# Performance work log

Hardware: AMD Instinct MI355X
Metric: run time of the kernel (lower is better)

The kernel has to match this reference:

```python
import jax, jax.numpy as jnp
import numpy as np

D_MODEL = 1024
D = 512
B = 32
L = 1024


def setup_inputs() -> dict:
    key = jax.random.key(0)
    ks = jax.random.split(key, 8)
    s = 1.0 / np.sqrt(D_MODEL)
    x = jax.random.normal(ks[0], (B, L, D_MODEL), dtype=jnp.float32)
    mask = jnp.ones((B, 1, L), dtype=jnp.int32)  # padding mask; 1 = keep
    Wq = jax.random.uniform(ks[1], (D, D_MODEL), jnp.float32, -s, s)
    bq = jax.random.uniform(ks[2], (D,), jnp.float32, -s, s)
    Wk = jax.random.uniform(ks[3], (D, D_MODEL), jnp.float32, -s, s)
    bk = jax.random.uniform(ks[4], (D,), jnp.float32, -s, s)
    Wv = jax.random.uniform(ks[5], (D, D_MODEL), jnp.float32, -s, s)
    bv = jax.random.uniform(ks[6], (D,), jnp.float32, -s, s)
    return {"x": x, "Wq": Wq, "bq": bq, "Wk": Wk, "bk": bk, "Wv": Wv, "bv": bv, "mask": mask}


def reference(x, Wq, bq, Wk, bk, Wv, bv, mask):
    Bq, Lq, _ = x.shape
    q = jnp.einsum('blc,dc->bld', x, Wq) + bq  # [B,L,D]
    k = jnp.einsum('blc,dc->bld', x, Wk) + bk
    v = jnp.einsum('blc,dc->bld', x, Wv) + bv
    scale = k.shape[-1] ** -0.5
    weights = jnp.einsum('bid,bjd->bij', q, k) * scale  # [B,L,L]
    causal = jnp.tril(jnp.ones((Lq, Lq), dtype=bool))
    neg_inf = jnp.float32(-jnp.inf)
    weights = jnp.where(causal[None, :, :], weights, neg_inf)
    weights = jnp.where(mask == 0, neg_inf, weights)  # mask broadcasts [B,1,L]
    weights = jax.nn.softmax(weights, axis=-1)
    # NOTE: source calls self.dropout(weights) but discards result -> no-op
    out = jnp.einsum('bij,bjd->bid', weights, v)
    return jax.nn.relu(out)
```

## Files before the change

### kernel.cpp

```cpp
#include <hip/hip_runtime.h>
#include <hip/hip_bf16.h>
#include <stdint.h>

#define DM 1024
#define DD 512
#define BB 32
#define LL 1024
#define SCALE 0.04419417382415922f
#define MAT ((size_t)BB * LL * DD)

typedef float f32x4 __attribute__((ext_vector_type(4)));
typedef short bf16x8 __attribute__((ext_vector_type(8)));
typedef short bf16x4 __attribute__((ext_vector_type(4)));

__device__ inline unsigned short f2bf(float f) {
    union { float f; uint32_t u; } v; v.f = f;
    uint32_t r = v.u + 0x7fffu + ((v.u >> 16) & 1u);
    return (unsigned short)(r >> 16);
}

__device__ inline bf16x4 cvt4(f32x4 a, float s) {
    bf16x4 r;
    r[0] = (short)f2bf(a[0] * s);
    r[1] = (short)f2bf(a[1] * s);
    r[2] = (short)f2bf(a[2] * s);
    r[3] = (short)f2bf(a[3] * s);
    return r;
}

#define GLOAD_LDS16(gsrc, ldst) \
    __builtin_amdgcn_global_load_lds((const __attribute__((address_space(1))) unsigned int*)(gsrc), \
        (__attribute__((address_space(3))) unsigned int*)(ldst), 16, 0, 0)

__device__ inline void tile_barrier() {
    asm volatile("s_waitcnt vmcnt(0)" ::: "memory");
    __builtin_amdgcn_sched_barrier(0);
    __builtin_amdgcn_s_barrier();
    __builtin_amdgcn_sched_barrier(0);
}

__global__ __launch_bounds__(256) void cast_x(const float* __restrict__ x,
                                              unsigned short* __restrict__ xb)
{
    size_t idx = (size_t)blockIdx.x * 256 + threadIdx.x;
    size_t base = idx * 8;
    f32x4 a = *(const f32x4*)(x + base);
    f32x4 b = *(const f32x4*)(x + base + 4);
    bf16x4 lo = cvt4(a, 1.0f), hi = cvt4(b, 1.0f);
    bf16x8 o = {lo[0], lo[1], lo[2], lo[3], hi[0], hi[1], hi[2], hi[3]};
    *(bf16x8*)(xb + base) = o;
}

__global__ __launch_bounds__(256) void cast_w(const float* __restrict__ Wq,
                                              const float* __restrict__ Wk,
                                              const float* __restrict__ Wv,
                                              unsigned short* __restrict__ Wb)
{
    size_t idx = (size_t)blockIdx.x * 256 + threadIdx.x;
    int o = (int)(idx >> 16);
    size_t rem = idx & 65535;
    const float* W = (o == 0) ? Wq : (o == 1) ? Wk : Wv;
    float s = (o == 0) ? SCALE : 1.0f;
    size_t base = rem * 8;
    f32x4 a = *(const f32x4*)(W + base);
    f32x4 b = *(const f32x4*)(W + base + 4);
    bf16x4 lo = cvt4(a, s), hi = cvt4(b, s);
    bf16x8 out = {lo[0], lo[1], lo[2], lo[3], hi[0], hi[1], hi[2], hi[3]};
    *(bf16x8*)(Wb + (size_t)o * 524288 + base) = out;
}

__global__ __launch_bounds__(256, 2) void qkv_proj3(
    const unsigned short* __restrict__ xb,
    const unsigned short* __restrict__ Wb,
    const float* __restrict__ bq, const float* __restrict__ bk, const float* __restrict__ bv,
    unsigned short* __restrict__ qkv)
{
    __shared__ __align__(16) unsigned short At[2][8192];
    __shared__ __align__(16) unsigned short Bt[2][8192];

    const int o = blockIdx.y;
    const float* bias = (o == 0) ? bq : (o == 1) ? bk : bv;
    const float wscale = (o == 0) ? SCALE : 1.0f;
    const unsigned short* W = Wb + (size_t)o * 524288;
    unsigned short* out = qkv + (size_t)o * MAT;

    int wg = blockIdx.x;
    wg = (wg & 7) * 128 + (wg >> 3);
    const int rowbase = (wg >> 2) * 128;
    const int colbase = (wg & 3) * 128;

    const int tid  = threadIdx.x;
    const int lane = tid & 63;
    const int w    = tid >> 6;
    const int wr   = (w >> 1) * 64;
    const int wc   = (w & 1) * 64;
    const int l15  = lane & 15, l4 = lane >> 4;

    const int r8   = lane >> 3;
    const int swch = (lane & 7) ^ r8;

    const char* xpanel = (const char*)(xb + (size_t)rowbase * DM);
    const char* wpanel = (const char*)(W  + (size_t)colbase * DM);

    f32x4 acc[4][4];
    #pragma unroll
    for (int i = 0; i < 4; ++i)
        #pragma unroll
        for (int j = 0; j < 4; ++j)
            acc[i][j] = (f32x4){0.f, 0.f, 0.f, 0.f};

    #define STAGE_AB(KK, BUF) do {                                               \
        _Pragma("unroll")                                                        \
        for (int i2 = 0; i2 < 4; ++i2) {                                         \
            int grp = i2 * 4 + w;                 \
            size_t rowoff = (size_t)(grp * 8 + r8) * 2048 + (KK) * 2 + swch * 16;\
            GLOAD_LDS16(xpanel + rowoff, (char*)&At[BUF][0] + grp * 1024);       \
            GLOAD_LDS16(wpanel + rowoff, (char*)&Bt[BUF][0] + grp * 1024);       \
        }                                                                        \
    } while (0)

    STAGE_AB(0, 0);
    __syncthreads();

    for (int t = 0; t < 16; ++t) {
        const int cur = t & 1;
        if (t < 15) STAGE_AB((t + 1) * 64, cur ^ 1);

        const char* Ab = (const char*)&At[cur][0];
        const char* Bb = (const char*)&Bt[cur][0];
        #pragma unroll
        for (int ks = 0; ks < 2; ++ks) {
            bf16x8 af[4], bf_[4];
            const int ch = (ks * 4 + l4) ^ (l15 & 7);
            #pragma unroll
            for (int m = 0; m < 4; ++m) {
                int row = wr + m * 16 + l15;
                af[m] = *(const bf16x8*)(Ab + row * 128 + (ch << 4));
            }
            #pragma unroll
            for (int n = 0; n < 4; ++n) {
                int row = wc + n * 16 + l15;
                bf_[n] = *(const bf16x8*)(Bb + row * 128 + (ch << 4));
            }
            #pragma unroll
            for (int n = 0; n < 4; ++n)
                #pragma unroll
                for (int m = 0; m < 4; ++m)
                    acc[m][n] = __builtin_amdgcn_mfma_f32_16x16x32_bf16(af[m], bf_[n], acc[m][n], 0, 0, 0);
        }

        if (t < 15) tile_barrier();
    }
    #undef STAGE_AB

    #pragma unroll
    for (int n = 0; n < 4; ++n) {
        int col = colbase + wc + n * 16 + l15;
        float bv_ = bias[col] * wscale;
        #pragma unroll
        for (int m = 0; m < 4; ++m) {
            int row0 = rowbase + wr + m * 16 + l4 * 4;
            #pragma unroll
            for (int r = 0; r < 4; ++r)
                out[(size_t)(row0 + r) * DD + col] = f2bf(acc[m][n][r] + bv_);
        }
    }
}

__global__ __launch_bounds__(256) void vtrans(const unsigned short* __restrict__ v,
                                              unsigned short* __restrict__ vt)
{
    __shared__ unsigned short T[64][72];
    const int lt = blockIdx.x, dt = blockIdx.y, b = blockIdx.z;
    const int t = threadIdx.x;
    const unsigned short* src = v + ((size_t)(b * LL + lt * 64)) * DD + dt * 64;
    #pragma unroll
    for (int it = 0; it < 2; ++it) {
        int r  = (t >> 3) + it * 32;
        int c0 = (t & 7) * 8;
        bf16x8 x = *(const bf16x8*)(src + (size_t)r * DD + c0);
        *(bf16x4*)&T[r][c0]     = (bf16x4){x[0], x[1], x[2], x[3]};
        *(bf16x4*)&T[r][c0 + 4] = (bf16x4){x[4], x[5], x[6], x[7]};
    }
    __syncthreads();
    unsigned short* dst = vt + ((size_t)(b * DD + dt * 64)) * LL + lt * 64;
    #pragma unroll
    for (int it = 0; it < 2; ++it) {
        int d  = (t >> 3) + it * 32;
        int c0 = (t & 7) * 8;
        bf16x8 o;
        #pragma unroll
        for (int e = 0; e < 8; ++e) o[e] = T[c0 + e][d];
        *(bf16x8*)(dst + (size_t)d * LL + c0) = o;
    }
}

__global__ __launch_bounds__(256, 1) void attn3(
    const unsigned short* __restrict__ qkv,
    const unsigned short* __restrict__ vt,
    const int* __restrict__ mask,
    float* __restrict__ outp)
{
    __shared__ __align__(16) unsigned short KtL[2][16384];
    __shared__ __align__(16) unsigned short VtL[2][16384];
    __shared__ __align__(16) unsigned short Pw[4][16][36];
    __shared__ float mbias[1024];

    const int bx = blockIdx.x;
    const int h = bx >> 8, i = bx & 255;
    const int b = i & 31;
    const int qtx = (i >> 5) & 7;
    const int qt = h ? qtx : 15 - qtx;

    const int tid = threadIdx.x, lane = tid & 63, w = tid >> 6;
    const int l15 = lane & 15, l4 = lane >> 4;
    const int lsw = lane * 16;

    const unsigned short* q = qkv;
    const unsigned short* k = qkv + MAT;
    const char* kb  = (const char*)k + ((size_t)b * LL) * DD * 2;
    const char* vtb = (const char*)vt + ((size_t)b * DD) * LL * 2;

    {
        const int* mp = mask + b * LL;
        #pragma unroll
        for (int j = 0; j < 4; ++j)
            mbias[tid * 4 + j] = mp[tid * 4 + j] ? 0.0f : -1e30f;
    }

    bf16x8 qf[16];
    {
        const unsigned short* qp = q + ((size_t)(b * LL + qt * 64 + w * 16 + l15)) * DD + l4 * 8;
        #pragma unroll
        for (int ks = 0; ks < 16; ++ks)
            qf[ks] = *(const bf16x8*)(qp + ks * 32);
    }

    f32x4 oacc[32];
    #pragma unroll
    for (int n = 0; n < 32; ++n) oacc[n] = (f32x4){0.f, 0.f, 0.f, 0.f};
    float mrow[4] = {-1e30f, -1e30f, -1e30f, -1e30f};
    float lrow[4] = {0.f, 0.f, 0.f, 0.f};

    const int jtmax = 2 * qt + 1;

    #define STAGE_KV(JT, BUF) do {                                              \
        const char* kt = kb + ((size_t)(JT) << 15);                             \
        char* ldsK = (char*)&KtL[(BUF)][0];                                     \
        _Pragma("unroll")                                                       \
        for (int i2 = 0; i2 < 8; ++i2) {                                        \
            int row = i2 * 4 + w;                                               \
            GLOAD_LDS16(kt + (row << 10) + (lsw ^ ((row & 7) << 4)),            \
                        ldsK + (row << 10));                                    \
        }                                                                       \
        const char* vtj = vtb + ((size_t)(JT) << 6);                            \
        char* ldsV = (char*)&VtL[(BUF)][0];                                     \
        _Pragma("unroll")                                                       \
        for (int i2 = 0; i2 < 8; ++i2) {                                        \
            int c0 = i2 * 256 + w * 64;                                         \
            int c  = c0 + lane;                                                 \
            GLOAD_LDS16(vtj + ((size_t)(c >> 2) << 11) + ((c & 3) << 4),        \
                        ldsV + c0 * 16);                                        \
        }                                                                       \
    } while (0)

    STAGE_KV(0, 0);
    __syncthreads();

    const int swz = (l15 & 7) << 4;

    for (int jt = 0; jt <= jtmax; ++jt) {
        const int cur = jt & 1;
        if (jt < jtmax) STAGE_KV(jt + 1, cur ^ 1);

        const char* Kc = (const char*)&KtL[cur][0];
        f32x4 sacc[2];
        sacc[0] = (f32x4){0.f, 0.f, 0.f, 0.f};
        sacc[1] = (f32x4){0.f, 0.f, 0.f, 0.f};
        #pragma unroll
        for (int ks = 0; ks < 16; ++ks) {
            int coloff = ((ks << 6) + (l4 << 4)) ^ swz;
            #pragma unroll
            for (int nf = 0; nf < 2; ++nf) {
                const bf16x8 kf = *(const bf16x8*)(Kc + ((nf * 16 + l15) << 10) + coloff);
                sacc[nf] = __builtin_amdgcn_mfma_f32_16x16x32_bf16(qf[ks], kf, sacc[nf], 0, 0, 0);
            }
        }

        const bool diag = (jt >= 2 * qt);
        float s[2][4];
        #pragma unroll
        for (int nf = 0; nf < 2; ++nf) {
            float bb_ = mbias[jt * 32 + nf * 16 + l15];
            #pragma unroll
            for (int r = 0; r < 4; ++r) {
                float val = sacc[nf][r] + bb_;
                if (diag) {
                    int gi = qt * 64 + w * 16 + l4 * 4 + r;
                    int gj = jt * 32 + nf * 16 + l15;
                    val = (gj <= gi) ? val : -3e38f;
                }
                s[nf][r] = val;
            }
        }
        float pm[4];
        #pragma unroll
        for (int r = 0; r < 4; ++r) {
            float mx = fmaxf(s[0][r], s[1][r]);
            mx = fmaxf(mx, __shfl_xor(mx, 1));
            mx = fmaxf(mx, __shfl_xor(mx, 2));
            mx = fmaxf(mx, __shfl_xor(mx, 4));
            mx = fmaxf(mx, __shfl_xor(mx, 8));
            pm[r] = mx;
        }
        bool need = false;
        #pragma unroll
        for (int r = 0; r < 4; ++r) need |= (pm[r] - mrow[r] > 8.0f);
        if (__any(need)) {
            #pragma unroll
            for (int r = 0; r < 4; ++r) {
                float mn = fmaxf(mrow[r], pm[r]);
                float corr = __expf(mrow[r] - mn);
                mrow[r] = mn;
                lrow[r] *= corr;
                #pragma unroll
                for (int n = 0; n < 32; ++n) oacc[n][r] *= corr;
            }
        }
        #pragma unroll
        for (int r = 0; r < 4; ++r) {
            float ls = 0.f;
            #pragma unroll
            for (int nf = 0; nf < 2; ++nf) {
                float p = __expf(s[nf][r] - mrow[r]);
                ls += p;
                Pw[w][l4 * 4 + r][nf * 16 + l15] = f2bf(p);
            }
            ls += __shfl_xor(ls, 1);
            ls += __shfl_xor(ls, 2);
            ls += __shfl_xor(ls, 4);
            ls += __shfl_xor(ls, 8);
            lrow[r] += ls;
        }

        const bf16x8 pa = *(const bf16x8*)&Pw[w][l15][l4 * 8];
        const char* Vc = (const char*)&VtL[cur][0];
        #pragma unroll
        for (int n = 0; n < 32; ++n) {
            const bf16x8 vb_ = *(const bf16x8*)(Vc + ((n * 16 + l15) << 6) + (l4 << 4));
            oacc[n] = __builtin_amdgcn_mfma_f32_16x16x32_bf16(pa, vb_, oacc[n], 0, 0, 0);
        }

        if (jt < jtmax) tile_barrier();
    }

    float inv[4];
    #pragma unroll
    for (int r = 0; r < 4; ++r) inv[r] = 1.0f / lrow[r];
    float* op = outp + ((size_t)(b * LL + qt * 64 + w * 16 + l4 * 4)) * DD + l15;
    #pragma unroll
    for (int n = 0; n < 32; ++n)
        #pragma unroll
        for (int r = 0; r < 4; ++r)
            op[(size_t)r * DD + n * 16] = fmaxf(oacc[n][r] * inv[r], 0.f);
    #undef STAGE_KV
}

extern "C" void kernel_launch(void* const* d_in, const int* in_sizes, int n_in,
                              void* d_out, int out_size, void* d_ws, size_t ws_size,
                              hipStream_t stream) {
    const float* x  = (const float*)d_in[0];
    const float* Wq = (const float*)d_in[1];
    const float* bq = (const float*)d_in[2];
    const float* Wk = (const float*)d_in[3];
    const float* bk = (const float*)d_in[4];
    const float* Wv = (const float*)d_in[5];
    const float* bv = (const float*)d_in[6];
    const int* mask = (const int*)d_in[7];

    unsigned short* qkv = (unsigned short*)d_ws;
    unsigned short* v   = qkv + 2 * MAT;
    unsigned short* vtp = qkv + 3 * MAT;
    unsigned short* Wb  = vtp;
    unsigned short* xb  = (unsigned short*)d_out;
    float* out = (float*)d_out;

    cast_x<<<16384, 256, 0, stream>>>(x, xb);
    cast_w<<<768, 256, 0, stream>>>(Wq, Wk, Wv, Wb);
    qkv_proj3<<<dim3(1024, 3), 256, 0, stream>>>(xb, Wb, bq, bk, bv, qkv);
    vtrans<<<dim3(16, 8, 32), 256, 0, stream>>>(v, vtp);
    attn3<<<dim3(512), 256, 0, stream>>>(qkv, vtp, mask, out);
}
```

Before: 290.8 us.

## Single-buffer K/V in LDS with staggered staging for two blocks per CU

The attention kernel drops its double-buffered K and V LDS tiles for single buffers, halving its LDS footprint. Launch bounds now request two blocks per CU, so all 512 blocks can be resident at once instead of running as two waves. To keep some overlap, the V tile is loaded while QK^T runs and the next K tile while P·V runs, with a barrier between phases. The risks are an extra barrier per iteration, lost intra-block prefetch depth, and possible register spills under the tighter per-wave VGPR budget.

```diff
diff --git a/kernel.cpp b/kernel.cpp
--- a/kernel.cpp
+++ b/kernel.cpp
@@ -32,7 +32,7 @@
     __builtin_amdgcn_global_load_lds((const __attribute__((address_space(1))) unsigned int*)(gsrc), \
         (__attribute__((address_space(3))) unsigned int*)(ldst), 16, 0, 0)
 
-__device__ inline void tile_barrier() {
+__device__ inline void publish_barrier() {
     asm volatile("s_waitcnt vmcnt(0)" ::: "memory");
     __builtin_amdgcn_sched_barrier(0);
     __builtin_amdgcn_s_barrier();
@@ -112,7 +112,7 @@
     #define STAGE_AB(KK, BUF) do {                                               \
         _Pragma("unroll")                                                        \
         for (int i2 = 0; i2 < 4; ++i2) {                                         \
-            int grp = i2 * 4 + w;                 \
+            int grp = i2 * 4 + w;                                                \
             size_t rowoff = (size_t)(grp * 8 + r8) * 2048 + (KK) * 2 + swch * 16;\
             GLOAD_LDS16(xpanel + rowoff, (char*)&At[BUF][0] + grp * 1024);       \
             GLOAD_LDS16(wpanel + rowoff, (char*)&Bt[BUF][0] + grp * 1024);       \
@@ -149,7 +149,7 @@
                     acc[m][n] = __builtin_amdgcn_mfma_f32_16x16x32_bf16(af[m], bf_[n], acc[m][n], 0, 0, 0);
         }
 
-        if (t < 15) tile_barrier();
+        if (t < 15) publish_barrier();
     }
     #undef STAGE_AB
 
@@ -195,14 +195,14 @@
     }
 }
 
-__global__ __launch_bounds__(256, 1) void attn3(
+__global__ __launch_bounds__(256, 2) void attn4(
     const unsigned short* __restrict__ qkv,
     const unsigned short* __restrict__ vt,
     const int* __restrict__ mask,
     float* __restrict__ outp)
 {
-    __shared__ __align__(16) unsigned short KtL[2][16384];
-    __shared__ __align__(16) unsigned short VtL[2][16384];
+    __shared__ __align__(16) unsigned short KtL[16384];
+    __shared__ __align__(16) unsigned short VtL[16384];
     __shared__ __align__(16) unsigned short Pw[4][16][36];
     __shared__ float mbias[1024];
 
@@ -244,36 +244,35 @@
 
     const int jtmax = 2 * qt + 1;
 
-    #define STAGE_KV(JT, BUF) do {                                              \
+    #define STAGE_K(JT) do {                                                    \
         const char* kt = kb + ((size_t)(JT) << 15);                             \
-        char* ldsK = (char*)&KtL[(BUF)][0];                                     \
         _Pragma("unroll")                                                       \
         for (int i2 = 0; i2 < 8; ++i2) {                                        \
             int row = i2 * 4 + w;                                               \
             GLOAD_LDS16(kt + (row << 10) + (lsw ^ ((row & 7) << 4)),            \
-                        ldsK + (row << 10));                                    \
+                        (char*)KtL + (row << 10));                              \
         }                                                                       \
+    } while (0)
+
+    #define STAGE_V(JT) do {                                                    \
         const char* vtj = vtb + ((size_t)(JT) << 6);                            \
-        char* ldsV = (char*)&VtL[(BUF)][0];                                     \
         _Pragma("unroll")                                                       \
         for (int i2 = 0; i2 < 8; ++i2) {                                        \
             int c0 = i2 * 256 + w * 64;                                         \
             int c  = c0 + lane;                                                 \
             GLOAD_LDS16(vtj + ((size_t)(c >> 2) << 11) + ((c & 3) << 4),        \
-                        ldsV + c0 * 16);                                        \
+                        (char*)VtL + c0 * 16);                                  \
         }                                                                       \
     } while (0)
 
-    STAGE_KV(0, 0);
-    __syncthreads();
+    STAGE_K(0);
 
     const int swz = (l15 & 7) << 4;
 
     for (int jt = 0; jt <= jtmax; ++jt) {
-        const int cur = jt & 1;
-        if (jt < jtmax) STAGE_KV(jt + 1, cur ^ 1);
-
-        const char* Kc = (const char*)&KtL[cur][0];
+        publish_barrier();
+        STAGE_V(jt);
+
         f32x4 sacc[2];
         sacc[0] = (f32x4){0.f, 0.f, 0.f, 0.f};
         sacc[1] = (f32x4){0.f, 0.f, 0.f, 0.f};
@@ -282,7 +281,7 @@
             int coloff = ((ks << 6) + (l4 << 4)) ^ swz;
             #pragma unroll
             for (int nf = 0; nf < 2; ++nf) {
-                const bf16x8 kf = *(const bf16x8*)(Kc + ((nf * 16 + l15) << 10) + coloff);
+                const bf16x8 kf = *(const bf16x8*)((const char*)KtL + ((nf * 16 + l15) << 10) + coloff);
                 sacc[nf] = __builtin_amdgcn_mfma_f32_16x16x32_bf16(qf[ks], kf, sacc[nf], 0, 0, 0);
             }
         }
@@ -343,15 +342,15 @@
             lrow[r] += ls;
         }
 
+        publish_barrier();
+        if (jt < jtmax) STAGE_K(jt + 1);
+
         const bf16x8 pa = *(const bf16x8*)&Pw[w][l15][l4 * 8];
-        const char* Vc = (const char*)&VtL[cur][0];
         #pragma unroll
         for (int n = 0; n < 32; ++n) {
-            const bf16x8 vb_ = *(const bf16x8*)(Vc + ((n * 16 + l15) << 6) + (l4 << 4));
+            const bf16x8 vb_ = *(const bf16x8*)((const char*)VtL + ((n * 16 + l15) << 6) + (l4 << 4));
             oacc[n] = __builtin_amdgcn_mfma_f32_16x16x32_bf16(pa, vb_, oacc[n], 0, 0, 0);
         }
-
-        if (jt < jtmax) tile_barrier();
     }
 
     float inv[4];
@@ -363,7 +362,8 @@
         #pragma unroll
         for (int r = 0; r < 4; ++r)
             op[(size_t)r * DD + n * 16] = fmaxf(oacc[n][r] * inv[r], 0.f);
-    #undef STAGE_KV
+    #undef STAGE_K
+    #undef STAGE_V
 }
 
 extern "C" void kernel_launch(void* const* d_in, const int* in_sizes, int n_in,
@@ -389,5 +389,5 @@
     cast_w<<<768, 256, 0, stream>>>(Wq, Wk, Wv, Wb);
     qkv_proj3<<<dim3(1024, 3), 256, 0, stream>>>(xb, Wb, bq, bk, bv, qkv);
     vtrans<<<dim3(16, 8, 32), 256, 0, stream>>>(v, vtp);
-    attn3<<<dim3(512), 256, 0, stream>>>(qkv, vtp, mask, out);
-}
+    attn4<<<dim3(512), 256, 0, stream>>>(qkv, vtp, mask, out);
+}
```

New measurement: 390.2 us. 34.2% more time.

## Restructure QKV projection into 256x256 tiles with 8 waves and staged half-tile pipeline

Applied to the files above, without the earlier changes.

Replaces the 128x128-tile, 4-wave QKV projection GEMM with a 256x256 tile computed by 8 waves, splitting each K-step's A and B panels into halves. The halves are loaded in a staggered order, gated by partial vmcnt waits and barriers, so MFMA work on one quarter of the output tile overlaps loads of the next K-step. The larger tile raises operand reuse and cuts global traffic per FLOP. The cost is more accumulator registers (32 f32x4 per thread), 64KB of LDS, fewer workgroups, and four barriers per iteration.

```diff
diff --git a/kernel.cpp b/kernel.cpp
--- a/kernel.cpp
+++ b/kernel.cpp
@@ -34,6 +34,36 @@
 
 __device__ inline void tile_barrier() {
     asm volatile("s_waitcnt vmcnt(0)" ::: "memory");
+    __builtin_amdgcn_sched_barrier(0);
+    __builtin_amdgcn_s_barrier();
+    __builtin_amdgcn_sched_barrier(0);
+}
+
+__device__ inline void gate6() {
+    asm volatile("s_waitcnt vmcnt(6)" ::: "memory");
+    __builtin_amdgcn_sched_barrier(0);
+    __builtin_amdgcn_s_barrier();
+    __builtin_amdgcn_sched_barrier(0);
+}
+__device__ inline void gate4() {
+    asm volatile("s_waitcnt vmcnt(4)" ::: "memory");
+    __builtin_amdgcn_sched_barrier(0);
+    __builtin_amdgcn_s_barrier();
+    __builtin_amdgcn_sched_barrier(0);
+}
+__device__ inline void gate2() {
+    asm volatile("s_waitcnt vmcnt(2)" ::: "memory");
+    __builtin_amdgcn_sched_barrier(0);
+    __builtin_amdgcn_s_barrier();
+    __builtin_amdgcn_sched_barrier(0);
+}
+__device__ inline void gate0() {
+    asm volatile("s_waitcnt vmcnt(0)" ::: "memory");
+    __builtin_amdgcn_sched_barrier(0);
+    __builtin_amdgcn_s_barrier();
+    __builtin_amdgcn_sched_barrier(0);
+}
+__device__ inline void gateB() {
     __builtin_amdgcn_sched_barrier(0);
     __builtin_amdgcn_s_barrier();
     __builtin_amdgcn_sched_barrier(0);
@@ -69,14 +99,14 @@
     *(bf16x8*)(Wb + (size_t)o * 524288 + base) = out;
 }
 
-__global__ __launch_bounds__(256, 2) void qkv_proj3(
+__global__ __launch_bounds__(512, 2) void qkv_proj4(
     const unsigned short* __restrict__ xb,
     const unsigned short* __restrict__ Wb,
     const float* __restrict__ bq, const float* __restrict__ bk, const float* __restrict__ bv,
     unsigned short* __restrict__ qkv)
 {
-    __shared__ __align__(16) unsigned short At[2][8192];
-    __shared__ __align__(16) unsigned short Bt[2][8192];
+    __shared__ __align__(16) unsigned short AL[2][2][8192];
+    __shared__ __align__(16) unsigned short BL[2][2][8192];
 
     const int o = blockIdx.y;
     const float* bias = (o == 0) ? bq : (o == 1) ? bk : bv;
@@ -85,16 +115,18 @@
     unsigned short* out = qkv + (size_t)o * MAT;
 
     int wg = blockIdx.x;
-    wg = (wg & 7) * 128 + (wg >> 3);
-    const int rowbase = (wg >> 2) * 128;
-    const int colbase = (wg & 3) * 128;
+    wg = (wg & 7) * 32 + (wg >> 3);
+    const int mt = wg >> 1, nt = wg & 1;
+    const int rowbase = mt * 256;
+    const int colbase = nt * 256;
 
     const int tid  = threadIdx.x;
     const int lane = tid & 63;
     const int w    = tid >> 6;
-    const int wr   = (w >> 1) * 64;
-    const int wc   = (w & 1) * 64;
+    const int wm   = w >> 2;
+    const int wn   = w & 3;
     const int l15  = lane & 15, l4 = lane >> 4;
+    const int rxor = l15 & 7;
 
     const int r8   = lane >> 3;
     const int swch = (lane & 7) ^ r8;
@@ -102,67 +134,110 @@
     const char* xpanel = (const char*)(xb + (size_t)rowbase * DM);
     const char* wpanel = (const char*)(W  + (size_t)colbase * DM);
 
-    f32x4 acc[4][4];
-    #pragma unroll
-    for (int i = 0; i < 4; ++i)
+    #define STAGE_HALF(panel, T, H, slot) do {                                   \
+        _Pragma("unroll")                                                        \
+        for (int i2 = 0; i2 < 2; ++i2) {                                         \
+            int grp = i2 * 8 + w;                                                \
+            GLOAD_LDS16((panel) + ((size_t)((H) * 128 + grp * 8 + r8) * 2048)    \
+                            + (size_t)(T) * 128 + swch * 16,                     \
+                        (char*)(slot) + grp * 1024);                             \
+        }                                                                        \
+    } while (0)
+
+    #define RDA(base, mf4, ks) (*(const bf16x8*)((base) + (wm * 64 + (mf4) * 16 + l15) * 128 \
+                            + ((((ks) * 4 + l4) ^ rxor) << 4)))
+    #define RDB(base, nfl, ks) (*(const bf16x8*)((base) + (wn * 32 + (nfl) * 16 + l15) * 128 \
+                            + ((((ks) * 4 + l4) ^ rxor) << 4)))
+
+    f32x4 acc[8][4];
+    #pragma unroll
+    for (int i = 0; i < 8; ++i)
         #pragma unroll
         for (int j = 0; j < 4; ++j)
             acc[i][j] = (f32x4){0.f, 0.f, 0.f, 0.f};
 
-    #define STAGE_AB(KK, BUF) do {                                               \
-        _Pragma("unroll")                                                        \
-        for (int i2 = 0; i2 < 4; ++i2) {                                         \
-            int grp = i2 * 4 + w;                 \
-            size_t rowoff = (size_t)(grp * 8 + r8) * 2048 + (KK) * 2 + swch * 16;\
-            GLOAD_LDS16(xpanel + rowoff, (char*)&At[BUF][0] + grp * 1024);       \
-            GLOAD_LDS16(wpanel + rowoff, (char*)&Bt[BUF][0] + grp * 1024);       \
-        }                                                                        \
-    } while (0)
-
-    STAGE_AB(0, 0);
-    __syncthreads();
+    bf16x8 aF[4][2], bF[4][2];
+
+    STAGE_HALF(xpanel, 0, 0, &AL[0][0][0]);
+    STAGE_HALF(wpanel, 0, 0, &BL[0][0][0]);
+    STAGE_HALF(wpanel, 0, 1, &BL[0][1][0]);
+    STAGE_HALF(xpanel, 0, 1, &AL[0][1][0]);
 
     for (int t = 0; t < 16; ++t) {
-        const int cur = t & 1;
-        if (t < 15) STAGE_AB((t + 1) * 64, cur ^ 1);
-
-        const char* Ab = (const char*)&At[cur][0];
-        const char* Bb = (const char*)&Bt[cur][0];
+        const int c = t & 1, cn = c ^ 1;
+        const char* A0b = (const char*)&AL[c][0][0];
+        const char* A1b = (const char*)&AL[c][1][0];
+        const char* B0b = (const char*)&BL[c][0][0];
+        const char* B1b = (const char*)&BL[c][1][0];
+        const bool st = (t < 15);
+
+        if (st) { STAGE_HALF(xpanel, t + 1, 0, &AL[cn][0][0]); gate6(); } else gate4();
         #pragma unroll
         for (int ks = 0; ks < 2; ++ks) {
-            bf16x8 af[4], bf_[4];
-            const int ch = (ks * 4 + l4) ^ (l15 & 7);
-            #pragma unroll
-            for (int m = 0; m < 4; ++m) {
-                int row = wr + m * 16 + l15;
-                af[m] = *(const bf16x8*)(Ab + row * 128 + (ch << 4));
-            }
-            #pragma unroll
-            for (int n = 0; n < 4; ++n) {
-                int row = wc + n * 16 + l15;
-                bf_[n] = *(const bf16x8*)(Bb + row * 128 + (ch << 4));
-            }
-            #pragma unroll
-            for (int n = 0; n < 4; ++n)
+            #pragma unroll
+            for (int mf = 0; mf < 4; ++mf) aF[mf][ks] = RDA(A0b, mf, ks);
+            bF[0][ks] = RDB(B0b, 0, ks);
+            bF[1][ks] = RDB(B0b, 1, ks);
+        }
+        #pragma unroll
+        for (int ks = 0; ks < 2; ++ks)
+            #pragma unroll
+            for (int nf = 0; nf < 2; ++nf)
                 #pragma unroll
-                for (int m = 0; m < 4; ++m)
-                    acc[m][n] = __builtin_amdgcn_mfma_f32_16x16x32_bf16(af[m], bf_[n], acc[m][n], 0, 0, 0);
-        }
-
-        if (t < 15) tile_barrier();
-    }
-    #undef STAGE_AB
-
-    #pragma unroll
-    for (int n = 0; n < 4; ++n) {
-        int col = colbase + wc + n * 16 + l15;
+                for (int mf = 0; mf < 4; ++mf)
+                    acc[mf][nf] = __builtin_amdgcn_mfma_f32_16x16x32_bf16(aF[mf][ks], bF[nf][ks], acc[mf][nf], 0, 0, 0);
+
+        if (st) { STAGE_HALF(wpanel, t + 1, 0, &BL[cn][0][0]); gate6(); } else gate2();
+        #pragma unroll
+        for (int ks = 0; ks < 2; ++ks) {
+            bF[2][ks] = RDB(B1b, 0, ks);
+            bF[3][ks] = RDB(B1b, 1, ks);
+        }
+        #pragma unroll
+        for (int ks = 0; ks < 2; ++ks)
+            #pragma unroll
+            for (int nf = 0; nf < 2; ++nf)
+                #pragma unroll
+                for (int mf = 0; mf < 4; ++mf)
+                    acc[mf][2 + nf] = __builtin_amdgcn_mfma_f32_16x16x32_bf16(aF[mf][ks], bF[2 + nf][ks], acc[mf][2 + nf], 0, 0, 0);
+
+        if (st) { STAGE_HALF(wpanel, t + 1, 1, &BL[cn][1][0]); gate6(); } else gate0();
+        #pragma unroll
+        for (int ks = 0; ks < 2; ++ks)
+            #pragma unroll
+            for (int mf = 0; mf < 4; ++mf) aF[mf][ks] = RDA(A1b, mf, ks);
+        #pragma unroll
+        for (int ks = 0; ks < 2; ++ks)
+            #pragma unroll
+            for (int nf = 0; nf < 2; ++nf)
+                #pragma unroll
+                for (int mf = 0; mf < 4; ++mf)
+                    acc[4 + mf][nf] = __builtin_amdgcn_mfma_f32_16x16x32_bf16(aF[mf][ks], bF[nf][ks], acc[4 + mf][nf], 0, 0, 0);
+
+        if (st) STAGE_HALF(xpanel, t + 1, 1, &AL[cn][1][0]);
+        gateB();
+        #pragma unroll
+        for (int ks = 0; ks < 2; ++ks)
+            #pragma unroll
+            for (int nf = 0; nf < 2; ++nf)
+                #pragma unroll
+                for (int mf = 0; mf < 4; ++mf)
+                    acc[4 + mf][2 + nf] = __builtin_amdgcn_mfma_f32_16x16x32_bf16(aF[mf][ks], bF[2 + nf][ks], acc[4 + mf][2 + nf], 0, 0, 0);
+    }
+    #undef STAGE_HALF
+    #undef RDA
+    #undef RDB
+
+    #pragma unroll
+    for (int nf = 0; nf < 4; ++nf) {
+        int col = colbase + ((nf < 2) ? wn * 32 + nf * 16 : 128 + wn * 32 + (nf - 2) * 16) + l15;
         float bv_ = bias[col] * wscale;
         #pragma unroll
-        for (int m = 0; m < 4; ++m) {
-            int row0 = rowbase + wr + m * 16 + l4 * 4;
+        for (int mf = 0; mf < 8; ++mf) {
+            int row0 = rowbase + ((mf < 4) ? wm * 64 + mf * 16 : 128 + wm * 64 + (mf - 4) * 16) + l4 * 4;
             #pragma unroll
             for (int r = 0; r < 4; ++r)
-                out[(size_t)(row0 + r) * DD + col] = f2bf(acc[m][n][r] + bv_);
+                out[(size_t)(row0 + r) * DD + col] = f2bf(acc[mf][nf][r] + bv_);
         }
     }
 }
@@ -387,7 +462,7 @@
 
     cast_x<<<16384, 256, 0, stream>>>(x, xb);
     cast_w<<<768, 256, 0, stream>>>(Wq, Wk, Wv, Wb);
-    qkv_proj3<<<dim3(1024, 3), 256, 0, stream>>>(xb, Wb, bq, bk, bv, qkv);
+    qkv_proj4<<<dim3(256, 3), 512, 0, stream>>>(xb, Wb, bq, bk, bv, qkv);
     vtrans<<<dim3(16, 8, 32), 256, 0, stream>>>(v, vtp);
     attn3<<<dim3(512), 256, 0, stream>>>(qkv, vtp, mask, out);
 }
```

Result: faster. 278.6 us (-4.2%).
